# Kernel tuning notes

Hardware: AMD Instinct MI355X
Metric: run time of the kernel (lower is better)

Reference implementation:

```python
import jax, jax.numpy as jnp
import numpy as np

NUM_HASHES = 10
GROUP = 2
K = 5


def _strip_att(x, conv_w, rvecs, horizontal):
    # x: [n, c, h, w]; conv_w: [group*k, c]; rvecs: [num_hashes, c]
    n, c, h, w = x.shape
    hw = h * w
    pad = K // 2

    # ---- LSH group selection (vectorized, no python batch loop) ----
    x_flat = x.reshape(n, c, hw).transpose(0, 2, 1)          # [n, hw, c]
    proj = jnp.einsum('ntc,hc->nth', x_flat, rvecs)          # [n, hw, num_hashes]
    codes = (proj > 0).astype(jnp.float32)
    pow2 = jnp.power(2.0, jnp.arange(NUM_HASHES, dtype=jnp.float32))
    dec = codes @ pow2                                       # [n, hw]
    order = jnp.argsort(dec, axis=1)                         # [n, hw]
    sorted_t = jnp.take_along_axis(x_flat, order[:, :, None], axis=1)  # [n, hw, c]

    # select_best_group: batch element with largest L2 norm, shared by all
    norms = jnp.linalg.norm(sorted_t.reshape(n, -1), axis=1)  # [n]
    best = jnp.argmax(norms)
    best_group = jnp.take(sorted_t, best, axis=0)             # [hw, c]
    bg = jnp.broadcast_to(best_group.T.reshape(1, c, h, w), (n, c, h, w))

    # ---- sigmoid-gated dynamic strip filter (1x1 conv) ----
    filt = jnp.einsum('oc,nchw->nohw', conv_w, bg)            # [n, group*K, h, w]
    filt = jax.nn.sigmoid(filt).reshape(n, GROUP, 1, K, hw)

    # ---- unfold (im2col) along the strip axis, reflect-padded ----
    if horizontal:
        xp = jnp.pad(x, ((0, 0), (0, 0), (0, 0), (pad, pad)), mode='reflect')
        windows = jnp.stack([xp[:, :, :, i:i + w] for i in range(K)], axis=2)  # [n,c,K,h,w]
    else:
        xp = jnp.pad(x, ((0, 0), (0, 0), (pad, pad), (0, 0)), mode='reflect')
        windows = jnp.stack([xp[:, :, i:i + h, :] for i in range(K)], axis=2)  # [n,c,K,h,w]
    xr = windows.reshape(n, GROUP, c // GROUP, K, hw)

    out = jnp.sum(xr * filt, axis=3).reshape(n, c, h, w)
    return out


def setup_inputs() -> dict:
    key = jax.random.key(0)
    ks = jax.random.split(key, 7)
    n, c, h, w = 4, 64, 256, 256
    return {
        'x': jax.random.normal(ks[0], (n, c, h, w), dtype=jnp.float32),
        'conv_h_w': jax.random.normal(ks[1], (GROUP * K, c), dtype=jnp.float32) * 0.1,
        'conv_w_w': jax.random.normal(ks[2], (GROUP * K, c), dtype=jnp.float32) * 0.1,
        'rvecs_h': jax.random.normal(ks[3], (NUM_HASHES, c), dtype=jnp.float32),
        'rvecs_w': jax.random.normal(ks[4], (NUM_HASHES, c), dtype=jnp.float32),
        'gamma': jax.random.normal(ks[5], (c,), dtype=jnp.float32),
        'beta': jax.random.normal(ks[6], (c,), dtype=jnp.float32),
    }


def reference(x, conv_h_w, conv_w_w, rvecs_h, rvecs_w, gamma, beta):
    out = _strip_att(x, conv_h_w, rvecs_h, horizontal=True)
    out = _strip_att(out, conv_w_w, rvecs_w, horizontal=False)
    return gamma[None, :, None, None] * out + x * beta[None, :, None, None]
```

## Files before the change

### kernel.cpp

```cpp
#include <hip/hip_runtime.h>

#define NB 4
#define C 64
#define H 256
#define W 256
#define HW (H * W)
#define NH 10
#define KK 5
#define NBINS 1024
#define CHUNK 256
#define NCHUNK (HW / CHUNK)

__global__ __launch_bounds__(256) void sumsq_kernel(const float* __restrict__ x,
                                                    float* __restrict__ part) {
    int bid = blockIdx.x;
    int b = bid >> 8, ch = bid & 255;
    const float4* p = reinterpret_cast<const float4*>(x + (size_t)b * C * HW) + (size_t)ch * 4096;
    float s = 0.f;
    for (int i = threadIdx.x; i < 4096; i += 256) {
        float4 v = p[i];
        s += v.x * v.x + v.y * v.y + v.z * v.z + v.w * v.w;
    }
    __shared__ float red[256];
    red[threadIdx.x] = s;
    __syncthreads();
    for (int off = 128; off; off >>= 1) {
        if (threadIdx.x < off) red[threadIdx.x] += red[threadIdx.x + off];
        __syncthreads();
    }
    if (threadIdx.x == 0) part[bid] = red[0];
}

__global__ __launch_bounds__(256) void hash_kernel(const float* __restrict__ Xall,
                                                   const float* __restrict__ part,
                                                   int per_batch,
                                                   const float* __restrict__ rvecs,
                                                   const float* __restrict__ cwg,
                                                   float* __restrict__ filtU,
                                                   int* __restrict__ dec,
                                                   int* __restrict__ hist) {
    __shared__ float tile[CHUNK][33];
    __shared__ float rv[NH * C];
    __shared__ float cw[NH * C];
    __shared__ int lhist[NBINS];
    __shared__ float4 red4[256];
    int t = threadIdx.x;
    for (int i = t; i < NH * C; i += 256) { rv[i] = rvecs[i]; cw[i] = cwg[i]; }
    for (int i = t; i < NBINS; i += 256) lhist[i] = 0;

    float4 ss = make_float4(0.f, 0.f, 0.f, 0.f);
    for (int i = t; i < per_batch; i += 256) {
        ss.x += part[0 * per_batch + i];
        ss.y += part[1 * per_batch + i];
        ss.z += part[2 * per_batch + i];
        ss.w += part[3 * per_batch + i];
    }
    red4[t] = ss;
    __syncthreads();
    for (int off = 128; off; off >>= 1) {
        if (t < off) {
            red4[t].x += red4[t + off].x;
            red4[t].y += red4[t + off].y;
            red4[t].z += red4[t + off].z;
            red4[t].w += red4[t + off].w;
        }
        __syncthreads();
    }
    float4 nm = red4[0];
    float nv[NB] = {nm.x, nm.y, nm.z, nm.w};
    int best = 0;
    float m = nv[0];
#pragma unroll
    for (int i = 1; i < NB; i++)
        if (nv[i] > m) { m = nv[i]; best = i; }

    const float* X = Xall + (size_t)best * C * HW;
    int p0 = blockIdx.x * CHUNK;
    float acc[NH], cacc[NH];
#pragma unroll
    for (int h2 = 0; h2 < NH; h2++) { acc[h2] = 0.f; cacc[h2] = 0.f; }

    for (int half = 0; half < 2; half++) {
        __syncthreads();
        for (int c = 0; c < 32; c++) tile[t][c] = X[(size_t)(half * 32 + c) * HW + p0 + t];
        __syncthreads();
        for (int c = 0; c < 32; c += 4) {
            float4 v = make_float4(tile[t][c], tile[t][c + 1], tile[t][c + 2], tile[t][c + 3]);
#pragma unroll
            for (int h2 = 0; h2 < NH; h2++) {
                const float* r = rv + h2 * C + half * 32 + c;
                const float* cc = cw + h2 * C + half * 32 + c;
                acc[h2] += v.x * r[0] + v.y * r[1] + v.z * r[2] + v.w * r[3];
                cacc[h2] += v.x * cc[0] + v.y * cc[1] + v.z * cc[2] + v.w * cc[3];
            }
        }
    }
    int d = 0;
#pragma unroll
    for (int h2 = 0; h2 < NH; h2++) d |= (acc[h2] > 0.f) ? (1 << h2) : 0;
    dec[p0 + t] = d;
    atomicAdd(&lhist[d], 1);

    float* fu = filtU + (size_t)(p0 + t) * 12;
    float s01 = 1.f / (1.f + expf(-cacc[0])), s1 = 1.f / (1.f + expf(-cacc[1]));
    float s2 = 1.f / (1.f + expf(-cacc[2])), s3 = 1.f / (1.f + expf(-cacc[3]));
    float s4 = 1.f / (1.f + expf(-cacc[4])), s5 = 1.f / (1.f + expf(-cacc[5]));
    float s6 = 1.f / (1.f + expf(-cacc[6])), s7 = 1.f / (1.f + expf(-cacc[7]));
    float s8 = 1.f / (1.f + expf(-cacc[8])), s9 = 1.f / (1.f + expf(-cacc[9]));
    *reinterpret_cast<float4*>(fu + 0) = make_float4(s01, s1, s2, s3);
    *reinterpret_cast<float4*>(fu + 4) = make_float4(s4, s5, s6, s7);
    *reinterpret_cast<float4*>(fu + 8) = make_float4(s8, s9, 0.f, 0.f);

    __syncthreads();
    for (int i = t; i < NBINS; i += 256) hist[(size_t)i * NCHUNK + blockIdx.x] = lhist[i];
}

__global__ __launch_bounds__(256) void scan1_kernel(int* __restrict__ hist,
                                                    int* __restrict__ bintot) {
    int t = threadIdx.x;
    int lane = t & 63;
    int b = blockIdx.x * 4 + (t >> 6);
    int4 v = *reinterpret_cast<int4*>(hist + (size_t)b * NCHUNK + lane * 4);
    int s0 = v.x;
    int s1 = s0 + v.y;
    int s2 = s1 + v.z;
    int s3 = s2 + v.w;
    int s = s3;
#pragma unroll
    for (int off = 1; off < 64; off <<= 1) {
        int nbr = __shfl_up(s, off);
        if (lane >= off) s += nbr;
    }
    int excl = s - s3;
    int4 o;
    o.x = excl;
    o.y = excl + s0;
    o.z = excl + s1;
    o.w = excl + s2;
    *reinterpret_cast<int4*>(hist + (size_t)b * NCHUNK + lane * 4) = o;
    if (lane == 63) bintot[b] = s;
}

__global__ __launch_bounds__(256) void scatter_kernel(const int* __restrict__ dec,
                                                      const int* __restrict__ hist,
                                                      const int* __restrict__ bintot,
                                                      int* __restrict__ order) {
    __shared__ int boffs[NBINS];
    __shared__ int wtot[4];
    __shared__ int keys[CHUNK];
    int t = threadIdx.x;
    int lane = t & 63;
    int w = t >> 6;
    int4 v = *reinterpret_cast<const int4*>(bintot + t * 4);
    int s0 = v.x, s1 = s0 + v.y, s2 = s1 + v.z, s3 = s2 + v.w;
    int s = s3;
#pragma unroll
    for (int off = 1; off < 64; off <<= 1) {
        int nbr = __shfl_up(s, off);
        if (lane >= off) s += nbr;
    }
    int excl = s - s3;
    if (lane == 63) wtot[w] = s;
    __syncthreads();
    int wbase = 0;
#pragma unroll
    for (int i = 0; i < 4; i++) wbase += (i < w) ? wtot[i] : 0;
    boffs[t * 4 + 0] = wbase + excl;
    boffs[t * 4 + 1] = wbase + excl + s0;
    boffs[t * 4 + 2] = wbase + excl + s1;
    boffs[t * 4 + 3] = wbase + excl + s2;

    int p0 = blockIdx.x * CHUNK;
    int k = dec[p0 + t];
    keys[t] = k;
    __syncthreads();
    int r = 0;
    for (int j = 0; j < t; j++) r += (keys[j] == k) ? 1 : 0;
    int dst = boffs[k] + hist[(size_t)k * NCHUNK + blockIdx.x] + r;
    order[dst] = p0 + t;
}

__global__ __launch_bounds__(256) void filtsig_kernel(const float* __restrict__ filtU,
                                                      const int* __restrict__ order,
                                                      float* __restrict__ filt) {
    int p = blockIdx.x * 256 + threadIdx.x;
    int orig = order[p];
    const float4* fu = reinterpret_cast<const float4*>(filtU + (size_t)orig * 12);
    float4 a = fu[0], b4 = fu[1], c4 = fu[2];
    float v[10] = {a.x, a.y, a.z, a.w, b4.x, b4.y, b4.z, b4.w, c4.x, c4.y};
#pragma unroll
    for (int h2 = 0; h2 < NH; h2++) filt[(size_t)h2 * HW + p] = v[h2];
}

__global__ __launch_bounds__(256) void convh_kernel(const float* __restrict__ X,
                                                    const float* __restrict__ filt,
                                                    float* __restrict__ out1,
                                                    float* __restrict__ part) {
    int bid = blockIdx.x;
    int rb = bid & 63;
    int c = (bid >> 6) & (C - 1);
    int n = bid >> 12;
    int g = c >> 5;
    int t = threadIdx.x;
    int x4 = (t & 63) * 4;
    int y = rb * 4 + (t >> 6);

    const float* src = X + (((size_t)n * C + c) * H + y) * W;
    float4 M = *reinterpret_cast<const float4*>(src + x4);
    float s0, s1, s6, s7;
    if (x4 > 0) {
        float4 L = *reinterpret_cast<const float4*>(src + x4 - 4);
        s0 = L.z; s1 = L.w;
    } else {
        s0 = M.z; s1 = M.y;
    }
    if (x4 < W - 4) {
        float4 R = *reinterpret_cast<const float4*>(src + x4 + 4);
        s6 = R.x; s7 = R.y;
    } else {
        s6 = M.z; s7 = M.y;
    }
    float s[8] = {s0, s1, M.x, M.y, M.z, M.w, s6, s7};

    const float* fb = filt + (size_t)g * KK * HW + (size_t)y * W + x4;
    float4 acc = make_float4(0.f, 0.f, 0.f, 0.f);
#pragma unroll
    for (int k = 0; k < KK; k++) {
        float4 f = *reinterpret_cast<const float4*>(fb + (size_t)k * HW);
        acc.x += s[k] * f.x;
        acc.y += s[k + 1] * f.y;
        acc.z += s[k + 2] * f.z;
        acc.w += s[k + 3] * f.w;
    }
    *reinterpret_cast<float4*>(out1 + (((size_t)n * C + c) * H + y) * W + x4) = acc;

    float ss = acc.x * acc.x + acc.y * acc.y + acc.z * acc.z + acc.w * acc.w;
#pragma unroll
    for (int off = 32; off; off >>= 1) ss += __shfl_down(ss, off);
    __shared__ float wred[4];
    if ((t & 63) == 0) wred[t >> 6] = ss;
    __syncthreads();
    if (t == 0) part[bid] = wred[0] + wred[1] + wred[2] + wred[3];
}

__global__ __launch_bounds__(256) void convv_kernel(const float* __restrict__ out1,
                                                    const float* __restrict__ filt,
                                                    const float* __restrict__ x,
                                                    const float* __restrict__ gamma,
                                                    const float* __restrict__ beta,
                                                    float* __restrict__ out) {
    int bid = blockIdx.x;
    int yc = bid & 3;
    int c = (bid >> 2) & (C - 1);
    int n = bid >> 8;
    int g = c >> 5;
    int t = threadIdx.x;
    int x4 = (t & 63) * 4;
    int ys = yc * 64 + (t >> 6) * 16;

    const float* plane = out1 + ((size_t)n * C + c) * HW;
    float4 win[KK];
#pragma unroll
    for (int i = 0; i < 4; i++) {
        int yy = ys - 2 + i;
        yy = yy < 0 ? -yy : yy;
        win[i] = *reinterpret_cast<const float4*>(plane + (size_t)yy * W + x4);
    }
    float gm = gamma[c], bt = beta[c];
    const float* fgb = filt + (size_t)g * KK * HW;
    for (int dy = 0; dy < 16; dy++) {
        int y = ys + dy;
        int yy = y + 2;
        yy = (yy >= H) ? (2 * H - 2 - yy) : yy;
        win[4] = *reinterpret_cast<const float4*>(plane + (size_t)yy * W + x4);
        const float* fb = fgb + (size_t)y * W + x4;
        float4 acc = make_float4(0.f, 0.f, 0.f, 0.f);
#pragma unroll
        for (int k = 0; k < KK; k++) {
            float4 f = *reinterpret_cast<const float4*>(fb + (size_t)k * HW);
            acc.x += win[k].x * f.x;
            acc.y += win[k].y * f.y;
            acc.z += win[k].z * f.z;
            acc.w += win[k].w * f.w;
        }
        size_t idx = (((size_t)n * C + c) * H + y) * W + x4;
        float4 xv = *reinterpret_cast<const float4*>(x + idx);
        float4 o;
        o.x = gm * acc.x + bt * xv.x;
        o.y = gm * acc.y + bt * xv.y;
        o.z = gm * acc.z + bt * xv.z;
        o.w = gm * acc.w + bt * xv.w;
        *reinterpret_cast<float4*>(out + idx) = o;
#pragma unroll
        for (int k = 0; k < 4; k++) win[k] = win[k + 1];
    }
}

extern "C" void kernel_launch(void* const* d_in, const int* in_sizes, int n_in,
                              void* d_out, int out_size, void* d_ws, size_t ws_size,
                              hipStream_t stream) {
    const float* x      = (const float*)d_in[0];
    const float* conv_h = (const float*)d_in[1];
    const float* conv_w = (const float*)d_in[2];
    const float* rv_h   = (const float*)d_in[3];
    const float* rv_w   = (const float*)d_in[4];
    const float* gamma  = (const float*)d_in[5];
    const float* beta   = (const float*)d_in[6];
    float* out = (float*)d_out;

    char* w = (char*)d_ws;
    size_t off = 0;
    float* out1   = (float*)(w + off); off += (size_t)NB * C * HW * 4;
    float* filtU  = (float*)(w + off); off += (size_t)HW * 12 * 4;
    float* filt   = (float*)(w + off); off += (size_t)NH * HW * 4;
    int*   dec    = (int*)  (w + off); off += (size_t)HW * 4;
    int*   order  = (int*)  (w + off); off += (size_t)HW * 4;
    int*   hist   = (int*)  (w + off); off += (size_t)NCHUNK * NBINS * 4;
    int*   bintot = (int*)  (w + off); off += 4096;
    float* part1  = (float*)(w + off); off += (size_t)NB * 256 * 4;
    float* part2  = (float*)(w + off); off += (size_t)NB * 4096 * 4;

    sumsq_kernel<<<NB * 256, 256, 0, stream>>>(x, part1);
    hash_kernel<<<NCHUNK, 256, 0, stream>>>(x, part1, 256, rv_h, conv_h, filtU, dec, hist);
    scan1_kernel<<<NBINS / 4, 256, 0, stream>>>(hist, bintot);
    scatter_kernel<<<NCHUNK, 256, 0, stream>>>(dec, hist, bintot, order);
    filtsig_kernel<<<HW / 256, 256, 0, stream>>>(filtU, order, filt);
    convh_kernel<<<NB * C * (H / 4), 256, 0, stream>>>(x, filt, out1, part2);

    hash_kernel<<<NCHUNK, 256, 0, stream>>>(out1, part2, 4096, rv_w, conv_w, filtU, dec, hist);
    scan1_kernel<<<NBINS / 4, 256, 0, stream>>>(hist, bintot);
    scatter_kernel<<<NCHUNK, 256, 0, stream>>>(dec, hist, bintot, order);
    filtsig_kernel<<<HW / 256, 256, 0, stream>>>(filtU, order, filt);
    convv_kernel<<<NB * C * (H / 64), 256, 0, stream>>>(out1, filt, x, gamma, beta, out);
}
```

Baseline: 151.5 us.

## Fuse filter permutation into scatter, vectorize norm reduce, split convv rows finer

The scatter kernel now writes the filter values for each pixel directly to their sorted destination. This removes the separate order buffer and the filtsig kernel launch, twice per call. The partial-norm reduction in the hash kernel now reads float4 instead of scalars. The vertical conv doubles its grid, with 8 rows per thread instead of 16, which raises parallelism at the cost of more halo reloads.

```diff
diff --git a/kernel.cpp b/kernel.cpp
--- a/kernel.cpp
+++ b/kernel.cpp
@@ -49,11 +49,16 @@
     for (int i = t; i < NBINS; i += 256) lhist[i] = 0;
 
     float4 ss = make_float4(0.f, 0.f, 0.f, 0.f);
-    for (int i = t; i < per_batch; i += 256) {
-        ss.x += part[0 * per_batch + i];
-        ss.y += part[1 * per_batch + i];
-        ss.z += part[2 * per_batch + i];
-        ss.w += part[3 * per_batch + i];
+    int q4 = per_batch >> 2;
+    for (int i = t; i < q4; i += 256) {
+        float4 a = *reinterpret_cast<const float4*>(part + 0 * per_batch + i * 4);
+        float4 b = *reinterpret_cast<const float4*>(part + 1 * per_batch + i * 4);
+        float4 c = *reinterpret_cast<const float4*>(part + 2 * per_batch + i * 4);
+        float4 d = *reinterpret_cast<const float4*>(part + 3 * per_batch + i * 4);
+        ss.x += a.x + a.y + a.z + a.w;
+        ss.y += b.x + b.y + b.z + b.w;
+        ss.z += c.x + c.y + c.z + c.w;
+        ss.w += d.x + d.y + d.z + d.w;
     }
     red4[t] = ss;
     __syncthreads();
@@ -144,7 +149,8 @@
 __global__ __launch_bounds__(256) void scatter_kernel(const int* __restrict__ dec,
                                                       const int* __restrict__ hist,
                                                       const int* __restrict__ bintot,
-                                                      int* __restrict__ order) {
+                                                      const float* __restrict__ filtU,
+                                                      float* __restrict__ filt) {
     __shared__ int boffs[NBINS];
     __shared__ int wtot[4];
     __shared__ int keys[CHUNK];
@@ -177,19 +183,12 @@
     int r = 0;
     for (int j = 0; j < t; j++) r += (keys[j] == k) ? 1 : 0;
     int dst = boffs[k] + hist[(size_t)k * NCHUNK + blockIdx.x] + r;
-    order[dst] = p0 + t;
-}
-
-__global__ __launch_bounds__(256) void filtsig_kernel(const float* __restrict__ filtU,
-                                                      const int* __restrict__ order,
-                                                      float* __restrict__ filt) {
-    int p = blockIdx.x * 256 + threadIdx.x;
-    int orig = order[p];
-    const float4* fu = reinterpret_cast<const float4*>(filtU + (size_t)orig * 12);
+
+    const float4* fu = reinterpret_cast<const float4*>(filtU + (size_t)(p0 + t) * 12);
     float4 a = fu[0], b4 = fu[1], c4 = fu[2];
-    float v[10] = {a.x, a.y, a.z, a.w, b4.x, b4.y, b4.z, b4.w, c4.x, c4.y};
-#pragma unroll
-    for (int h2 = 0; h2 < NH; h2++) filt[(size_t)h2 * HW + p] = v[h2];
+    float vv[10] = {a.x, a.y, a.z, a.w, b4.x, b4.y, b4.z, b4.w, c4.x, c4.y};
+#pragma unroll
+    for (int h2 = 0; h2 < NH; h2++) filt[(size_t)h2 * HW + dst] = vv[h2];
 }
 
 __global__ __launch_bounds__(256) void convh_kernel(const float* __restrict__ X,
@@ -250,13 +249,13 @@
                                                     const float* __restrict__ beta,
                                                     float* __restrict__ out) {
     int bid = blockIdx.x;
-    int yc = bid & 3;
-    int c = (bid >> 2) & (C - 1);
-    int n = bid >> 8;
+    int yc = bid & 7;
+    int c = (bid >> 3) & (C - 1);
+    int n = bid >> 9;
     int g = c >> 5;
     int t = threadIdx.x;
     int x4 = (t & 63) * 4;
-    int ys = yc * 64 + (t >> 6) * 16;
+    int ys = yc * 32 + (t >> 6) * 8;
 
     const float* plane = out1 + ((size_t)n * C + c) * HW;
     float4 win[KK];
@@ -268,7 +267,7 @@
     }
     float gm = gamma[c], bt = beta[c];
     const float* fgb = filt + (size_t)g * KK * HW;
-    for (int dy = 0; dy < 16; dy++) {
+    for (int dy = 0; dy < 8; dy++) {
         int y = ys + dy;
         int yy = y + 2;
         yy = (yy >= H) ? (2 * H - 2 - yy) : yy;
@@ -314,7 +313,6 @@
     float* filtU  = (float*)(w + off); off += (size_t)HW * 12 * 4;
     float* filt   = (float*)(w + off); off += (size_t)NH * HW * 4;
     int*   dec    = (int*)  (w + off); off += (size_t)HW * 4;
-    int*   order  = (int*)  (w + off); off += (size_t)HW * 4;
     int*   hist   = (int*)  (w + off); off += (size_t)NCHUNK * NBINS * 4;
     int*   bintot = (int*)  (w + off); off += 4096;
     float* part1  = (float*)(w + off); off += (size_t)NB * 256 * 4;
@@ -323,13 +321,11 @@
     sumsq_kernel<<<NB * 256, 256, 0, stream>>>(x, part1);
     hash_kernel<<<NCHUNK, 256, 0, stream>>>(x, part1, 256, rv_h, conv_h, filtU, dec, hist);
     scan1_kernel<<<NBINS / 4, 256, 0, stream>>>(hist, bintot);
-    scatter_kernel<<<NCHUNK, 256, 0, stream>>>(dec, hist, bintot, order);
-    filtsig_kernel<<<HW / 256, 256, 0, stream>>>(filtU, order, filt);
+    scatter_kernel<<<NCHUNK, 256, 0, stream>>>(dec, hist, bintot, filtU, filt);
     convh_kernel<<<NB * C * (H / 4), 256, 0, stream>>>(x, filt, out1, part2);
 
     hash_kernel<<<NCHUNK, 256, 0, stream>>>(out1, part2, 4096, rv_w, conv_w, filtU, dec, hist);
     scan1_kernel<<<NBINS / 4, 256, 0, stream>>>(hist, bintot);
-    scatter_kernel<<<NCHUNK, 256, 0, stream>>>(dec, hist, bintot, order);
-    filtsig_kernel<<<HW / 256, 256, 0, stream>>>(filtU, order, filt);
-    convv_kernel<<<NB * C * (H / 64), 256, 0, stream>>>(out1, filt, x, gamma, beta, out);
-}
+    scatter_kernel<<<NCHUNK, 256, 0, stream>>>(dec, hist, bintot, filtU, filt);
+    convv_kernel<<<NB * C * 8, 256, 0, stream>>>(out1, filt, x, gamma, beta, out);
+}
```

Measured after the change: 149.0 us. No clear change (-1.6%).
